# Optimization experiments

Hardware: AMD Instinct MI355X
Metric: run time of the kernel (lower is better)

## Reference

```python
import jax, jax.numpy as jnp
import numpy as np

N, E, K, H, F_IN, F_OUT, Q = 50000, 1600000, 4, 4, 32, 32, 1


def setup_inputs() -> dict:
    key = jax.random.key(0)
    ks = jax.random.split(key, 5)
    x = jax.random.normal(ks[0], (N, H, F_IN, Q), dtype=jnp.float32)
    edge_index = jax.random.randint(ks[1], (2, E), 0, N, dtype=jnp.int64)
    edge_weight = jax.random.uniform(ks[2], (E,), dtype=jnp.float32)
    stdv = 1.0 / np.sqrt(F_IN * K)
    weight = jax.random.uniform(ks[3], (K, H, F_IN, F_OUT), dtype=jnp.float32, minval=-stdv, maxval=stdv)
    bias = jax.random.uniform(ks[4], (F_OUT,), dtype=jnp.float32, minval=-stdv, maxval=stdv)
    return {"x": x, "edge_index": edge_index, "edge_weight": edge_weight, "weight": weight, "bias": bias}


def reference(x, edge_index, edge_weight, weight, bias):
    # x: (n, h, f, q); weight: (K, h, f, g); edge_index: (2, E)
    n = x.shape[0]
    row, col = edge_index[0], edge_index[1]
    # remove_self_loops: zero out self-loop edges (static shapes, same math)
    mask = row != col
    ew = jnp.where(mask, edge_weight, jnp.zeros((), x.dtype))
    deg = jax.ops.segment_sum(mask.astype(x.dtype), row, num_segments=n)
    dinv = jnp.where(deg > 0, deg ** -0.5, jnp.zeros((), x.dtype))
    lap = -dinv[row] * ew * dinv[col]  # (E,)

    def spmm(t):
        # out[row] += lap * t[col]; t: (n, h, f, q)
        return jax.ops.segment_sum(lap[:, None, None, None] * t[col], row, num_segments=n)

    Kk = weight.shape[0]
    Tx0 = x
    out = jnp.einsum('nhfq,hfg->ngq', Tx0, weight[0])
    Tx1 = spmm(Tx0)
    out = out + jnp.einsum('nhfq,hfg->ngq', Tx1, weight[1])
    for k in range(2, Kk):
        Tx2 = 2.0 * spmm(Tx1) - Tx0
        out = out + jnp.einsum('nhfq,hfg->ngq', Tx2, weight[k])
        Tx0, Tx1 = Tx1, Tx2
    out = out[:, None]  # (n, 1, g, q) per collapse_H unsqueeze
    out = out + bias.reshape(1, 1, -1, 1)
    return out
```

## Files before the change

kernel.cpp:

```cpp
#include <hip/hip_runtime.h>


#define FEAT 128
#define GOUT 32
#define NCH 4
#define CHF 32
#define SCB 256
#define CH 4096
#define WCAP 16384
#define CAP 12032
#define TROW 160
#define UNR 8

typedef unsigned int uint;
typedef unsigned short ushort;

__device__ __forceinline__ ushort f2bf(float f) {
    uint u = __float_as_uint(f);
    return (ushort)((u + 0x7fffu + ((u >> 16) & 1u)) >> 16);
}
__device__ __forceinline__ float bflo(uint u) { return __uint_as_float(u << 16); }
__device__ __forceinline__ float bfhi(uint u) { return __uint_as_float(u & 0xffff0000u); }
__device__ __forceinline__ int tidx(int i) { return i + ((i >> 4) << 2); }

__global__ __launch_bounds__(1024) void bin_kernel(
    const int* __restrict__ ei, const float* __restrict__ ew, int E,
    int* __restrict__ bucketCursor, uint2* __restrict__ staging) {
    __shared__ int hist[256];
    __shared__ int base[256];
    int e0 = blockIdx.x * CH;
    int t = threadIdx.x;
    if (t < 256) hist[t] = 0;
    __syncthreads();
    int r[4], c[4];
    float wv[4];
#pragma unroll
    for (int k = 0; k < 4; ++k) {
        int e = e0 + k * 1024 + t;
        r[k] = -1;
        if (e < E) {
            int rr = ei[e], cc = ei[(size_t)E + e];
            wv[k] = ew[e];
            if (rr != cc) {
                r[k] = rr; c[k] = cc;
                atomicAdd(&hist[rr >> 8], 1);
            }
        }
    }
    __syncthreads();
    if (t < 256) {
        int h = hist[t];
        if (h > 0) {
            int run = atomicAdd(&bucketCursor[t], h);
            base[t] = t * CAP + run;
        }
        hist[t] = 0;
    }
    __syncthreads();
#pragma unroll
    for (int k = 0; k < 4; ++k) {
        if (r[k] >= 0) {
            int bk = r[k] >> 8;
            int j = atomicAdd(&hist[bk], 1);
            int idx = base[bk] + j;
            if (idx < (bk + 1) * CAP)
                staging[idx] = make_uint2(__float_as_uint(wv[k]),
                                          ((uint)c[k] << 16) | (uint)(r[k] & 255));
        }
    }
}

__global__ __launch_bounds__(256) void bucket_count_kernel(
    const uint2* __restrict__ staging, const int* __restrict__ bucketCursor,
    int* __restrict__ cnt, int n) {
    __shared__ int hist[256];
    int b = blockIdx.x;
    int t = threadIdx.x;
    hist[t] = 0;
    __syncthreads();
    int nrec = bucketCursor[b];
    const uint2* src = staging + (size_t)b * CAP;
    for (int k = t; k < nrec; k += 256)
        atomicAdd(&hist[src[k].y & 255], 1);
    __syncthreads();
    int r = (b << 8) + t;
    if (r < n) cnt[r] = hist[t];
}

__global__ void scan1_kernel(const int* __restrict__ cnt, int* __restrict__ partial,
                             int* __restrict__ blockSums, float* __restrict__ dinv, int n) {
    __shared__ int buf[2][SCB];
    int t = threadIdx.x;
    int i = blockIdx.x * SCB + t;
    int v = (i < n) ? cnt[i] : 0;
    if (i < n) dinv[i] = (v > 0) ? rsqrtf((float)v) : 0.0f;
    buf[0][t] = v;
    __syncthreads();
    int src = 0;
    for (int off = 1; off < SCB; off <<= 1) {
        int d = src ^ 1;
        buf[d][t] = buf[src][t] + ((t >= off) ? buf[src][t - off] : 0);
        __syncthreads();
        src = d;
    }
    int incl = buf[src][t];
    if (i < n) partial[i] = incl - v;
    if (t == SCB - 1) blockSums[blockIdx.x] = incl;
}

__global__ void scan2_kernel(const int* __restrict__ blockSums, int* __restrict__ blockOffsets,
                             int nb, int* __restrict__ total_out) {
    __shared__ int buf[2][SCB];
    __shared__ int carry_s;
    if (threadIdx.x == 0) carry_s = 0;
    __syncthreads();
    for (int base = 0; base < nb; base += SCB) {
        int i = base + (int)threadIdx.x;
        int v = (i < nb) ? blockSums[i] : 0;
        buf[0][threadIdx.x] = v;
        __syncthreads();
        int src = 0;
        for (int off = 1; off < SCB; off <<= 1) {
            int d = src ^ 1;
            buf[d][threadIdx.x] = buf[src][threadIdx.x] +
                                  ((threadIdx.x >= (unsigned)off) ? buf[src][threadIdx.x - off] : 0);
            __syncthreads();
            src = d;
        }
        int incl = buf[src][threadIdx.x];
        int c = carry_s;
        if (i < nb) blockOffsets[i] = c + incl - v;
        __syncthreads();
        if (threadIdx.x == SCB - 1) carry_s = c + incl;
        __syncthreads();
    }
    if (threadIdx.x == 0) *total_out = carry_s;
}

__global__ void scan3_kernel(const int* __restrict__ partial, const int* __restrict__ blockOffsets,
                             int* __restrict__ offsets, int n) {
    int i = blockIdx.x * blockDim.x + threadIdx.x;
    if (i < n) offsets[i] = partial[i] + blockOffsets[i / SCB];
}

__global__ __launch_bounds__(256) void scatter_kernel(
    const uint2* __restrict__ staging, const int* __restrict__ bucketCursor,
    const int* __restrict__ offsets, const float* __restrict__ dinv,
    uint* __restrict__ csr, int n) {
    __shared__ uint win[WCAP];
    __shared__ int roff[256];
    __shared__ int rcur[256];
    __shared__ float dloc[256];
    int b = blockIdx.x;
    int r0 = b << 8;
    int nrows = min(256, n - r0);
    int t = threadIdx.x;
    if (t < nrows) {
        roff[t] = offsets[r0 + t];
        dloc[t] = dinv[r0 + t];
    }
    rcur[t] = 0;
    __syncthreads();
    int wbeg = roff[0];
    int nrec = bucketCursor[b];
    bool fit = (nrec <= WCAP);
    const uint2* src = staging + (size_t)b * CAP;
    for (int k = t; k < nrec; k += 256) {
        uint2 rec = src[k];
        int col = rec.y >> 16;
        int rl = rec.y & 255;
        float lap = -dloc[rl] * __uint_as_float(rec.x) * dinv[col];
        uint colap = ((uint)col << 16) | (uint)f2bf(lap);
        int pos = roff[rl] + atomicAdd(&rcur[rl], 1);
        if (fit) win[pos - wbeg] = colap;
        else csr[pos] = colap;
    }
    __syncthreads();
    if (fit)
        for (int k = t; k < nrec; k += 256) csr[wbeg + k] = win[k];
}

__global__ __launch_bounds__(256) void cvt_einsum0_kernel(
    const float* __restrict__ x, ushort* __restrict__ xb,
    const float* __restrict__ W0, const float* __restrict__ bias,
    float* __restrict__ out, int n) {
    __shared__ __align__(16) float4 sW4[FEAT * GOUT / 4];
    __shared__ __align__(16) float sT[8 * TROW];
    const float* sW = (const float*)sW4;
    int t = threadIdx.x;
    const float4* wsrc = (const float4*)W0;
    for (int idx = t; idx < FEAT * GOUT / 4; idx += 256) sW4[idx] = wsrc[idx];
    int node = blockIdx.x * 8 + (t >> 5);
    int f0 = 4 * (t & 31);
    float4 v = make_float4(0.f, 0.f, 0.f, 0.f);
    if (node < n) {
        v = *(const float4*)(x + (size_t)node * FEAT + f0);
        ushort4 o;
        o.x = f2bf(v.x); o.y = f2bf(v.y); o.z = f2bf(v.z); o.w = f2bf(v.w);
        int j0 = f0 >> 5;
        *(ushort4*)(xb + ((size_t)j0 * n + node) * CHF + (f0 & 31)) = o;
    }
    int nl = t >> 5;
    *(float4*)&sT[nl * TROW + tidx(f0)] = v;
    __syncthreads();
    int l32 = t & 31;
    int q = l32 & 7;
    int part = l32 >> 3;
    float4 a4 = make_float4(0.f, 0.f, 0.f, 0.f);
#pragma unroll
    for (int j = 0; j < 8; ++j) {
        float4 t4 = *(const float4*)&sT[nl * TROW + tidx(part * 32 + 4 * j)];
        const float* wv0 = &sW[(part * 32 + 4 * j) * GOUT + 4 * q];
        float4 w0 = *(const float4*)(wv0);
        float4 w1 = *(const float4*)(wv0 + GOUT);
        float4 w2 = *(const float4*)(wv0 + 2 * GOUT);
        float4 w3 = *(const float4*)(wv0 + 3 * GOUT);
        a4.x += t4.x * w0.x + t4.y * w1.x + t4.z * w2.x + t4.w * w3.x;
        a4.y += t4.x * w0.y + t4.y * w1.y + t4.z * w2.y + t4.w * w3.y;
        a4.z += t4.x * w0.z + t4.y * w1.z + t4.z * w2.z + t4.w * w3.z;
        a4.w += t4.x * w0.w + t4.y * w1.w + t4.z * w2.w + t4.w * w3.w;
    }
    a4.x += __shfl_down(a4.x, 8);  a4.y += __shfl_down(a4.y, 8);
    a4.z += __shfl_down(a4.z, 8);  a4.w += __shfl_down(a4.w, 8);
    a4.x += __shfl_down(a4.x, 16); a4.y += __shfl_down(a4.y, 16);
    a4.z += __shfl_down(a4.z, 16); a4.w += __shfl_down(a4.w, 16);
    if (part == 0 && node < n) {
        const float4 b4 = *(const float4*)(bias + 4 * q);
        float4 r;
        r.x = a4.x + b4.x; r.y = a4.y + b4.y; r.z = a4.z + b4.z; r.w = a4.w + b4.w;
        *(float4*)(out + (size_t)node * GOUT + 4 * q) = r;
    }
}

__global__ __launch_bounds__(512) void spmm_chunk_kernel(
    const ushort* __restrict__ inb, const ushort* __restrict__ sub,
    ushort* __restrict__ outb, const int* __restrict__ offsets,
    const uint* __restrict__ csr, const float* __restrict__ Wk,
    float* __restrict__ out, int n, int has_sub, int write_out, int nbj) {
    __shared__ __align__(16) float sW[CHF * GOUT];
    __shared__ float sT2[8][8][CHF + 1];
    int j = blockIdx.x / nbj;
    int b = blockIdx.x % nbj;
    int t = threadIdx.x;
    const float4* wsrc = (const float4*)(Wk + j * CHF * GOUT);
    for (int i2 = t; i2 < CHF * GOUT / 4; i2 += 512) ((float4*)sW)[i2] = wsrc[i2];
    __syncthreads();
    int w = t >> 6, lane = t & 63, s = lane >> 3, u = lane & 7;
    int node = b * 64 + w * 8 + s;
    bool alive = node < n;
    int beg = 0, deg = 0;
    if (alive) { beg = offsets[node]; deg = offsets[node + 1] - beg; }
    int m = deg;
    m = max(m, __shfl_xor(m, 8));
    m = max(m, __shfl_xor(m, 16));
    m = max(m, __shfl_xor(m, 32));
    const uint2* inb_u2 = (const uint2*)inb;
    size_t jb2 = (size_t)j * n * 8;
    size_t obase = jb2 + (size_t)node * 8 + u;
    uint2 sv = make_uint2(0u, 0u);
    if (has_sub && alive) sv = ((const uint2*)sub)[obase];
    float a0 = 0.f, a1 = 0.f, a2 = 0.f, a3 = 0.f;
    uint q[UNR];
    uint2 uu[UNR];
#pragma unroll
    for (int k = 0; k < UNR; ++k)
        q[k] = (k < deg) ? csr[beg + k] : 0u;
#pragma unroll
    for (int k = 0; k < UNR; ++k)
        uu[k] = inb_u2[jb2 + (size_t)(q[k] >> 16) * 8 + u];
    for (int it = 0; it < m; it += UNR) {
        uint qn[UNR];
        uint2 un[UNR];
        int nx = it + UNR;
#pragma unroll
        for (int k = 0; k < UNR; ++k)
            qn[k] = (nx + k < deg) ? csr[beg + nx + k] : 0u;
#pragma unroll
        for (int k = 0; k < UNR; ++k)
            un[k] = inb_u2[jb2 + (size_t)(qn[k] >> 16) * 8 + u];
#pragma unroll
        for (int k = 0; k < UNR; ++k) {
            float l = bflo(q[k]);
            a0 += l * bflo(uu[k].x);
            a1 += l * bfhi(uu[k].x);
            a2 += l * bflo(uu[k].y);
            a3 += l * bfhi(uu[k].y);
        }
#pragma unroll
        for (int k = 0; k < UNR; ++k) { q[k] = qn[k]; uu[k] = un[k]; }
    }
    if (has_sub) {
        a0 = 2.f * a0 - bflo(sv.x);
        a1 = 2.f * a1 - bfhi(sv.x);
        a2 = 2.f * a2 - bflo(sv.y);
        a3 = 2.f * a3 - bfhi(sv.y);
    }
    if (alive && write_out) {
        uint2 o;
        o.x = (uint)f2bf(a0) | ((uint)f2bf(a1) << 16);
        o.y = (uint)f2bf(a2) | ((uint)f2bf(a3) << 16);
        ((uint2*)outb)[obase] = o;
    }
    sT2[w][s][4 * u + 0] = a0;
    sT2[w][s][4 * u + 1] = a1;
    sT2[w][s][4 * u + 2] = a2;
    sT2[w][s][4 * u + 3] = a3;
    __builtin_amdgcn_wave_barrier();
    float e0 = 0.f, e1 = 0.f, e2 = 0.f, e3 = 0.f;
#pragma unroll
    for (int i = 0; i < CHF; ++i) {
        float tv = sT2[w][s][i];
        e0 += tv * sW[i * GOUT + u];
        e1 += tv * sW[i * GOUT + u + 8];
        e2 += tv * sW[i * GOUT + u + 16];
        e3 += tv * sW[i * GOUT + u + 24];
    }
    if (alive) {
        float* po = out + (size_t)node * GOUT;
        atomicAdd(po + u, e0);
        atomicAdd(po + u + 8, e1);
        atomicAdd(po + u + 16, e2);
        atomicAdd(po + u + 24, e3);
    }
}

extern "C" void kernel_launch(void* const* d_in, const int* in_sizes, int n_in,
                              void* d_out, int out_size, void* d_ws, size_t ws_size,
                              hipStream_t stream) {
    const float* x = (const float*)d_in[0];
    const int* ei = (const int*)d_in[1];
    const float* ew = (const float*)d_in[2];
    const float* W = (const float*)d_in[3];
    const float* bias = (const float*)d_in[4];
    float* out = (float*)d_out;

    const int N = in_sizes[0] / FEAT;
    const int E = in_sizes[1] / 2;
    const int NB = (N + SCB - 1) / SCB;
    const int NBUK = (N + 255) >> 8;
    const int NBJ = (((N + 63) / 64 + 7) / 8) * 8;

    char* p = (char*)d_ws;
    auto alloc = [&](size_t bytes) {
        char* q = p;
        p += (bytes + 255) & ~(size_t)255;
        return q;
    };
    int* cnt = (int*)alloc((size_t)N * 4);
    int* offsets = (int*)alloc(((size_t)N + 1) * 4);
    float* dinv = (float*)alloc((size_t)N * 4);
    int* partial = (int*)alloc((size_t)N * 4);
    int* blockSums = (int*)alloc((size_t)NB * 4);
    int* blockOffsets = (int*)alloc((size_t)NB * 4);
    int* bucketCursor = (int*)alloc((size_t)NBUK * 4);
    uint* csr = (uint*)alloc(((size_t)E + 64) * 4);
    ushort* xb = (ushort*)alloc((size_t)N * FEAT * 2);
    ushort* Ab = (ushort*)alloc((size_t)N * FEAT * 2);
    ushort* Bb = (ushort*)alloc((size_t)N * FEAT * 2);
    uint2* staging = (uint2*)Ab;
    (void)ws_size;

    hipMemsetAsync(bucketCursor, 0, (size_t)NBUK * 4, stream);

    bin_kernel<<<(E + CH - 1) / CH, 1024, 0, stream>>>(ei, ew, E, bucketCursor, staging);
    bucket_count_kernel<<<NBUK, 256, 0, stream>>>(staging, bucketCursor, cnt, N);
    scan1_kernel<<<NB, SCB, 0, stream>>>(cnt, partial, blockSums, dinv, N);
    scan2_kernel<<<1, SCB, 0, stream>>>(blockSums, blockOffsets, NB, offsets + N);
    scan3_kernel<<<NB, SCB, 0, stream>>>(partial, blockOffsets, offsets, N);
    scatter_kernel<<<NBUK, 256, 0, stream>>>(staging, bucketCursor, offsets, dinv, csr, N);

    cvt_einsum0_kernel<<<(N + 7) / 8, 256, 0, stream>>>(x, xb, W, bias, out, N);

    dim3 sg(NCH * NBJ);
    spmm_chunk_kernel<<<sg, 512, 0, stream>>>(xb, nullptr, Ab, offsets, csr,
                                              W + 1 * FEAT * GOUT, out, N, 0, 1, NBJ);
    spmm_chunk_kernel<<<sg, 512, 0, stream>>>(Ab, xb, Bb, offsets, csr,
                                              W + 2 * FEAT * GOUT, out, N, 1, 1, NBJ);
    spmm_chunk_kernel<<<sg, 512, 0, stream>>>(Bb, Ab, nullptr, offsets, csr,
                                              W + 3 * FEAT * GOUT, out, N, 1, 0, NBJ);
}
```

Baseline: 359.8 us.

## Fuse CSR build kernels, shrink bin blocks, drop gather prefetch in SpMM

Merges bucket counting with the first scan stage and folds the final offset scan into the scatter kernel, cutting two launches and a round trip through the cnt and offsets arrays. The bin kernel now uses 512-thread blocks over 2048-edge chunks, which gives more blocks and less atomic contention per block. The SpMM loop no longer prefetches the next batch of gathered features across iterations. That lowers register pressure but leaves the gather latency less hidden. Bucket record counts are also clamped to CAP when read.

```diff
diff --git a/kernel.cpp b/kernel.cpp
--- a/kernel.cpp
+++ b/kernel.cpp
@@ -5,8 +5,7 @@
 #define GOUT 32
 #define NCH 4
 #define CHF 32
-#define SCB 256
-#define CH 4096
+#define CH 2048
 #define WCAP 16384
 #define CAP 12032
 #define TROW 160
@@ -23,7 +22,7 @@
 __device__ __forceinline__ float bfhi(uint u) { return __uint_as_float(u & 0xffff0000u); }
 __device__ __forceinline__ int tidx(int i) { return i + ((i >> 4) << 2); }
 
-__global__ __launch_bounds__(1024) void bin_kernel(
+__global__ __launch_bounds__(512) void bin_kernel(
     const int* __restrict__ ei, const float* __restrict__ ew, int E,
     int* __restrict__ bucketCursor, uint2* __restrict__ staging) {
     __shared__ int hist[256];
@@ -36,7 +35,7 @@
     float wv[4];
 #pragma unroll
     for (int k = 0; k < 4; ++k) {
-        int e = e0 + k * 1024 + t;
+        int e = e0 + k * 512 + t;
         r[k] = -1;
         if (e < E) {
             int rr = ei[e], cc = ei[(size_t)E + e];
@@ -70,57 +69,51 @@
     }
 }
 
-__global__ __launch_bounds__(256) void bucket_count_kernel(
+__global__ __launch_bounds__(256) void bc_scan1_kernel(
     const uint2* __restrict__ staging, const int* __restrict__ bucketCursor,
-    int* __restrict__ cnt, int n) {
+    int* __restrict__ partial, int* __restrict__ blockSums,
+    float* __restrict__ dinv, int n) {
     __shared__ int hist[256];
+    __shared__ int buf[2][256];
     int b = blockIdx.x;
     int t = threadIdx.x;
     hist[t] = 0;
     __syncthreads();
-    int nrec = bucketCursor[b];
+    int nrec = min(bucketCursor[b], CAP);
     const uint2* src = staging + (size_t)b * CAP;
     for (int k = t; k < nrec; k += 256)
         atomicAdd(&hist[src[k].y & 255], 1);
     __syncthreads();
-    int r = (b << 8) + t;
-    if (r < n) cnt[r] = hist[t];
-}
-
-__global__ void scan1_kernel(const int* __restrict__ cnt, int* __restrict__ partial,
-                             int* __restrict__ blockSums, float* __restrict__ dinv, int n) {
-    __shared__ int buf[2][SCB];
-    int t = threadIdx.x;
-    int i = blockIdx.x * SCB + t;
-    int v = (i < n) ? cnt[i] : 0;
+    int v = hist[t];
+    int i = (b << 8) + t;
     if (i < n) dinv[i] = (v > 0) ? rsqrtf((float)v) : 0.0f;
     buf[0][t] = v;
     __syncthreads();
-    int src = 0;
-    for (int off = 1; off < SCB; off <<= 1) {
-        int d = src ^ 1;
-        buf[d][t] = buf[src][t] + ((t >= off) ? buf[src][t - off] : 0);
+    int srcb = 0;
+    for (int off = 1; off < 256; off <<= 1) {
+        int d = srcb ^ 1;
+        buf[d][t] = buf[srcb][t] + ((t >= off) ? buf[srcb][t - off] : 0);
         __syncthreads();
-        src = d;
-    }
-    int incl = buf[src][t];
+        srcb = d;
+    }
+    int incl = buf[srcb][t];
     if (i < n) partial[i] = incl - v;
-    if (t == SCB - 1) blockSums[blockIdx.x] = incl;
+    if (t == 255) blockSums[b] = incl;
 }
 
 __global__ void scan2_kernel(const int* __restrict__ blockSums, int* __restrict__ blockOffsets,
                              int nb, int* __restrict__ total_out) {
-    __shared__ int buf[2][SCB];
+    __shared__ int buf[2][256];
     __shared__ int carry_s;
     if (threadIdx.x == 0) carry_s = 0;
     __syncthreads();
-    for (int base = 0; base < nb; base += SCB) {
+    for (int base = 0; base < nb; base += 256) {
         int i = base + (int)threadIdx.x;
         int v = (i < nb) ? blockSums[i] : 0;
         buf[0][threadIdx.x] = v;
         __syncthreads();
         int src = 0;
-        for (int off = 1; off < SCB; off <<= 1) {
+        for (int off = 1; off < 256; off <<= 1) {
             int d = src ^ 1;
             buf[d][threadIdx.x] = buf[src][threadIdx.x] +
                                   ((threadIdx.x >= (unsigned)off) ? buf[src][threadIdx.x - off] : 0);
@@ -131,21 +124,16 @@
         int c = carry_s;
         if (i < nb) blockOffsets[i] = c + incl - v;
         __syncthreads();
-        if (threadIdx.x == SCB - 1) carry_s = c + incl;
+        if (threadIdx.x == 255) carry_s = c + incl;
         __syncthreads();
     }
     if (threadIdx.x == 0) *total_out = carry_s;
-}
-
-__global__ void scan3_kernel(const int* __restrict__ partial, const int* __restrict__ blockOffsets,
-                             int* __restrict__ offsets, int n) {
-    int i = blockIdx.x * blockDim.x + threadIdx.x;
-    if (i < n) offsets[i] = partial[i] + blockOffsets[i / SCB];
 }
 
 __global__ __launch_bounds__(256) void scatter_kernel(
     const uint2* __restrict__ staging, const int* __restrict__ bucketCursor,
-    const int* __restrict__ offsets, const float* __restrict__ dinv,
+    const int* __restrict__ partial, const int* __restrict__ blockOffsets,
+    const float* __restrict__ dinv, int* __restrict__ offsets,
     uint* __restrict__ csr, int n) {
     __shared__ uint win[WCAP];
     __shared__ int roff[256];
@@ -153,16 +141,18 @@
     __shared__ float dloc[256];
     int b = blockIdx.x;
     int r0 = b << 8;
-    int nrows = min(256, n - r0);
-    int t = threadIdx.x;
-    if (t < nrows) {
-        roff[t] = offsets[r0 + t];
-        dloc[t] = dinv[r0 + t];
+    int t = threadIdx.x;
+    int i = r0 + t;
+    if (i < n) {
+        int o = partial[i] + blockOffsets[b];
+        roff[t] = o;
+        offsets[i] = o;
+        dloc[t] = dinv[i];
     }
     rcur[t] = 0;
     __syncthreads();
     int wbeg = roff[0];
-    int nrec = bucketCursor[b];
+    int nrec = min(bucketCursor[b], CAP);
     bool fit = (nrec <= WCAP);
     const uint2* src = staging + (size_t)b * CAP;
     for (int k = t; k < nrec; k += 256) {
@@ -261,23 +251,19 @@
     if (has_sub && alive) sv = ((const uint2*)sub)[obase];
     float a0 = 0.f, a1 = 0.f, a2 = 0.f, a3 = 0.f;
     uint q[UNR];
-    uint2 uu[UNR];
 #pragma unroll
     for (int k = 0; k < UNR; ++k)
         q[k] = (k < deg) ? csr[beg + k] : 0u;
-#pragma unroll
-    for (int k = 0; k < UNR; ++k)
-        uu[k] = inb_u2[jb2 + (size_t)(q[k] >> 16) * 8 + u];
     for (int it = 0; it < m; it += UNR) {
+        uint2 uu[UNR];
+#pragma unroll
+        for (int k = 0; k < UNR; ++k)
+            uu[k] = inb_u2[jb2 + (size_t)(q[k] >> 16) * 8 + u];
         uint qn[UNR];
-        uint2 un[UNR];
         int nx = it + UNR;
 #pragma unroll
         for (int k = 0; k < UNR; ++k)
             qn[k] = (nx + k < deg) ? csr[beg + nx + k] : 0u;
-#pragma unroll
-        for (int k = 0; k < UNR; ++k)
-            un[k] = inb_u2[jb2 + (size_t)(qn[k] >> 16) * 8 + u];
 #pragma unroll
         for (int k = 0; k < UNR; ++k) {
             float l = bflo(q[k]);
@@ -287,7 +273,7 @@
             a3 += l * bfhi(uu[k].y);
         }
 #pragma unroll
-        for (int k = 0; k < UNR; ++k) { q[k] = qn[k]; uu[k] = un[k]; }
+        for (int k = 0; k < UNR; ++k) q[k] = qn[k];
     }
     if (has_sub) {
         a0 = 2.f * a0 - bflo(sv.x);
@@ -336,7 +322,6 @@
 
     const int N = in_sizes[0] / FEAT;
     const int E = in_sizes[1] / 2;
-    const int NB = (N + SCB - 1) / SCB;
     const int NBUK = (N + 255) >> 8;
     const int NBJ = (((N + 63) / 64 + 7) / 8) * 8;
 
@@ -346,12 +331,11 @@
         p += (bytes + 255) & ~(size_t)255;
         return q;
     };
-    int* cnt = (int*)alloc((size_t)N * 4);
     int* offsets = (int*)alloc(((size_t)N + 1) * 4);
     float* dinv = (float*)alloc((size_t)N * 4);
     int* partial = (int*)alloc((size_t)N * 4);
-    int* blockSums = (int*)alloc((size_t)NB * 4);
-    int* blockOffsets = (int*)alloc((size_t)NB * 4);
+    int* blockSums = (int*)alloc((size_t)NBUK * 4);
+    int* blockOffsets = (int*)alloc((size_t)NBUK * 4);
     int* bucketCursor = (int*)alloc((size_t)NBUK * 4);
     uint* csr = (uint*)alloc(((size_t)E + 64) * 4);
     ushort* xb = (ushort*)alloc((size_t)N * FEAT * 2);
@@ -362,12 +346,12 @@
 
     hipMemsetAsync(bucketCursor, 0, (size_t)NBUK * 4, stream);
 
-    bin_kernel<<<(E + CH - 1) / CH, 1024, 0, stream>>>(ei, ew, E, bucketCursor, staging);
-    bucket_count_kernel<<<NBUK, 256, 0, stream>>>(staging, bucketCursor, cnt, N);
-    scan1_kernel<<<NB, SCB, 0, stream>>>(cnt, partial, blockSums, dinv, N);
-    scan2_kernel<<<1, SCB, 0, stream>>>(blockSums, blockOffsets, NB, offsets + N);
-    scan3_kernel<<<NB, SCB, 0, stream>>>(partial, blockOffsets, offsets, N);
-    scatter_kernel<<<NBUK, 256, 0, stream>>>(staging, bucketCursor, offsets, dinv, csr, N);
+    bin_kernel<<<(E + CH - 1) / CH, 512, 0, stream>>>(ei, ew, E, bucketCursor, staging);
+    bc_scan1_kernel<<<NBUK, 256, 0, stream>>>(staging, bucketCursor, partial,
+                                              blockSums, dinv, N);
+    scan2_kernel<<<1, 256, 0, stream>>>(blockSums, blockOffsets, NBUK, offsets + N);
+    scatter_kernel<<<NBUK, 256, 0, stream>>>(staging, bucketCursor, partial,
+                                             blockOffsets, dinv, offsets, csr, N);
 
     cvt_einsum0_kernel<<<(N + 7) / 8, 256, 0, stream>>>(x, xb, W, bias, out, N);
 
```

Result: no change. 357.7 us (-0.6%).
